# Optimization experiments

Hardware: AMD Instinct MI355X
Metric: run time of the kernel (lower is better)

## Reference

```python
import jax, jax.numpy as jnp
import numpy as np

N, T, V = 256, 70, 64
B, H, C = 6, 1024, 4  # n_blocks, n_internal_units, n_class
SPECTRAL_RADIUS = 0.99
INPUT_SCALING = 0.2


def setup_inputs() -> dict:
    key = jax.random.key(0)
    k1, k2, k3, k4 = jax.random.split(key, 4)
    X = jax.random.normal(k1, (N, T, V), dtype=jnp.float32)
    # spectral-radius-normalized reservoir weights (circular law: rho(G/sqrt(H)) ~ 1)
    W_res = jax.random.normal(k2, (B, H, H), dtype=jnp.float32) * (SPECTRAL_RADIUS / jnp.sqrt(H).astype(jnp.float32))
    # +/-1 Bernoulli input weights scaled by input_scaling
    W_in = jnp.sign(jax.random.normal(k3, (B, H, V), dtype=jnp.float32)) * INPUT_SCALING
    W_lin = jax.random.normal(k4, (T, C, B * H), dtype=jnp.float32) * 0.02
    b_lin = jnp.zeros((T, C), dtype=jnp.float32)
    return {"X": X, "W_res": W_res, "W_in": W_in, "W_lin": W_lin, "b_lin": b_lin}


def reference(X, W_res, W_in, W_lin, b_lin):
    # Echo state recurrence: s_t = tanh(W_res @ s_{t-1} + W_in @ x_t), per block
    # (leak=None, noise_level=0.0, n_drop=0 as in module defaults)
    n, t_len, v = X.shape
    b, h, _ = W_res.shape

    def step(s, x_t):  # s: [B,N,H], x_t: [N,V]
        pre = jnp.einsum('bij,bnj->bni', W_res, s) + jnp.einsum('bhv,nv->bnh', W_in, x_t)
        s_new = jnp.tanh(pre)
        return s_new, s_new

    s0 = jnp.zeros((b, n, h), dtype=X.dtype)
    _, states = jax.lax.scan(step, s0, jnp.swapaxes(X, 0, 1))  # [T,B,N,H]

    # per-timestep features: concat blocks -> [T,N,B*H]
    feats = jnp.transpose(states, (0, 2, 1, 3)).reshape(t_len, n, b * h)
    # per-timestep linear heads
    logits = jnp.einsum('tnf,tcf->tnc', feats, W_lin) + b_lin[:, None, :]  # [T,N,C]
    preds = jnp.argmax(logits, axis=-1)  # [T,N], matches forward()'s class_dict
    return logits, preds
```

## Files before the change

kernel.cpp:

```cpp
#include <hip/hip_runtime.h>
#include <stdint.h>


typedef _Float16 f16;
typedef _Float16 f16x8 __attribute__((ext_vector_type(8)));
typedef float floatx4 __attribute__((ext_vector_type(4)));

#define N_TOT 256
#define T_TOT 70
#define V_TOT 64
#define B_TOT 6
#define H_TOT 1024
#define C_TOT 4
#define F_TOT (B_TOT * H_TOT)
#define G_TOT 192
#define LDA 72
#define LO_SCALE 4096.0f
#define LO_INV   (1.0f / 4096.0f)

union H8 { f16 h[8]; uint4 v; };

__global__ __launch_bounds__(256)
void split_f32(const float* __restrict__ src, f16* __restrict__ hi,
               f16* __restrict__ lo, int n)
{
    const int i = (blockIdx.x * 256 + threadIdx.x) * 8;
    if (i + 8 > n) return;
    const float4 a = *(const float4*)&src[i];
    const float4 b = *(const float4*)&src[i + 4];
    const float x[8] = {a.x, a.y, a.z, a.w, b.x, b.y, b.z, b.w};
    H8 H, L;
#pragma unroll
    for (int j = 0; j < 8; ++j) {
        const f16 h = (f16)x[j];
        H.h[j] = h;
        L.h[j] = (f16)((x[j] - (float)h) * LO_SCALE);
    }
    *(uint4*)&hi[i] = H.v;
    *(uint4*)&lo[i] = L.v;
}

__global__ __launch_bounds__(256)
void head_reduce(const float* __restrict__ part,
                 const float* __restrict__ b_lin,
                 float* __restrict__ logits,
                 float* __restrict__ preds)
{
    const int t = blockIdx.x;
    const int n = threadIdx.x;

    float a0 = b_lin[t * C_TOT + 0];
    float a1 = b_lin[t * C_TOT + 1];
    float a2 = b_lin[t * C_TOT + 2];
    float a3 = b_lin[t * C_TOT + 3];

    const float* p = part + (((size_t)t * G_TOT) * N_TOT + n) * C_TOT;
    for (int g = 0; g < G_TOT; ++g) {
        const float4 v = *(const float4*)&p[(size_t)g * N_TOT * C_TOT];
        a0 += v.x; a1 += v.y; a2 += v.z; a3 += v.w;
    }

    float4 o = {a0, a1, a2, a3};
    *(float4*)&logits[((size_t)t * N_TOT + n) * C_TOT] = o;

    int arg = 0;
    float best = a0;
    if (a1 > best) { best = a1; arg = 1; }
    if (a2 > best) { best = a2; arg = 2; }
    if (a3 > best) { best = a3; arg = 3; }
    preds[(size_t)t * N_TOT + n] = (float)arg;
}

__global__ __launch_bounds__(256)
void esn_step_fused(const f16* __restrict__ Xhi,   const f16* __restrict__ Xlo,
                    const f16* __restrict__ Whi,   const f16* __restrict__ Wlo,
                    const f16* __restrict__ Wihi,  const f16* __restrict__ Wilo,
                    const f16* __restrict__ shi_p, const f16* __restrict__ slo_p,
                    f16* __restrict__ shi_n,       f16* __restrict__ slo_n,
                    const float* __restrict__ W_lin, float* __restrict__ part,
                    int t, int first)
{
    __shared__ f16 As_hi[64 * LDA];
    __shared__ f16 As_lo[64 * LDA];
    __shared__ f16 Bs_hi[32 * LDA];
    __shared__ f16 Bs_lo[32 * LDA];

    const int p   = blockIdx.x;
    const int l   = (p & 7) * 96 + (p >> 3);
    const int mt  = l & 3;
    const int bi  = l >> 2;
    const int b   = bi >> 5;
    const int it  = bi & 31;

    const int tid  = threadIdx.x;
    const int wm   = tid >> 6;
    const int lane = tid & 63;
    const int l16  = lane & 15;
    const int oct  = lane >> 4;

    const int ra = tid >> 2;
    const int ca = (tid & 3) << 4;
    const int rb = tid >> 3;
    const int cb = (tid & 7) << 3;

    floatx4 acc[2], accl[2];
#pragma unroll
    for (int j = 0; j < 2; ++j) { acc[j] = (floatx4)(0.0f); accl[j] = (floatx4)(0.0f); }

    if (!first) {
        const f16* Ah = shi_p + (size_t)(b * N_TOT + mt * 64 + ra) * H_TOT + ca;
        const f16* Al = slo_p + (size_t)(b * N_TOT + mt * 64 + ra) * H_TOT + ca;
        const f16* Bh = Whi   + (size_t)(b * H_TOT + it * 32 + rb) * H_TOT + cb;
        const f16* Bl = Wlo   + (size_t)(b * H_TOT + it * 32 + rb) * H_TOT + cb;

        uint4 pah0, pah1, pal0, pal1, pbh, pbl;
#define LOAD_CHUNK(J0)                                   \
        do {                                             \
            pah0 = *(const uint4*)&Ah[(J0) + 0];         \
            pah1 = *(const uint4*)&Ah[(J0) + 8];         \
            pal0 = *(const uint4*)&Al[(J0) + 0];         \
            pal1 = *(const uint4*)&Al[(J0) + 8];         \
            pbh  = *(const uint4*)&Bh[(J0)];             \
            pbl  = *(const uint4*)&Bl[(J0)];             \
        } while (0)

        LOAD_CHUNK(0);
        for (int kc = 0; kc < 16; ++kc) {
            if (kc) __syncthreads();
            *(uint4*)&As_hi[ra * LDA + ca]     = pah0;
            *(uint4*)&As_hi[ra * LDA + ca + 8] = pah1;
            *(uint4*)&As_lo[ra * LDA + ca]     = pal0;
            *(uint4*)&As_lo[ra * LDA + ca + 8] = pal1;
            *(uint4*)&Bs_hi[rb * LDA + cb]     = pbh;
            *(uint4*)&Bs_lo[rb * LDA + cb]     = pbl;
            __syncthreads();
            if (kc < 15) LOAD_CHUNK((kc + 1) * 64);

#pragma unroll
            for (int kk = 0; kk < 64; kk += 32) {
                const int ar = (wm * 16 + l16) * LDA + kk + oct * 8;
                const f16x8 ah = *(const f16x8*)&As_hi[ar];
                const f16x8 al = *(const f16x8*)&As_lo[ar];
#pragma unroll
                for (int nf = 0; nf < 2; ++nf) {
                    const int br = (nf * 16 + l16) * LDA + kk + oct * 8;
                    const f16x8 bh = *(const f16x8*)&Bs_hi[br];
                    const f16x8 bl = *(const f16x8*)&Bs_lo[br];
                    acc[nf]  = __builtin_amdgcn_mfma_f32_16x16x32_f16(ah, bh, acc[nf], 0, 0, 0);
                    accl[nf] = __builtin_amdgcn_mfma_f32_16x16x32_f16(ah, bl, accl[nf], 0, 0, 0);
                    accl[nf] = __builtin_amdgcn_mfma_f32_16x16x32_f16(al, bh, accl[nf], 0, 0, 0);
                }
            }
        }
#undef LOAD_CHUNK
        __syncthreads();
    }

    {
        const size_t xb = ((size_t)(mt * 64 + ra) * T_TOT + t) * V_TOT + ca;
        *(uint4*)&As_hi[ra * LDA + ca]     = *(const uint4*)&Xhi[xb];
        *(uint4*)&As_hi[ra * LDA + ca + 8] = *(const uint4*)&Xhi[xb + 8];
        *(uint4*)&As_lo[ra * LDA + ca]     = *(const uint4*)&Xlo[xb];
        *(uint4*)&As_lo[ra * LDA + ca + 8] = *(const uint4*)&Xlo[xb + 8];
        const size_t wb = (size_t)(b * H_TOT + it * 32 + rb) * V_TOT + cb;
        *(uint4*)&Bs_hi[rb * LDA + cb] = *(const uint4*)&Wihi[wb];
        *(uint4*)&Bs_lo[rb * LDA + cb] = *(const uint4*)&Wilo[wb];
        __syncthreads();
#pragma unroll
        for (int kk = 0; kk < 64; kk += 32) {
            const int ar = (wm * 16 + l16) * LDA + kk + oct * 8;
            const f16x8 ah = *(const f16x8*)&As_hi[ar];
            const f16x8 al = *(const f16x8*)&As_lo[ar];
#pragma unroll
            for (int nf = 0; nf < 2; ++nf) {
                const int br = (nf * 16 + l16) * LDA + kk + oct * 8;
                const f16x8 bh = *(const f16x8*)&Bs_hi[br];
                const f16x8 bl = *(const f16x8*)&Bs_lo[br];
                acc[nf]  = __builtin_amdgcn_mfma_f32_16x16x32_f16(ah, bh, acc[nf], 0, 0, 0);
                accl[nf] = __builtin_amdgcn_mfma_f32_16x16x32_f16(ah, bl, accl[nf], 0, 0, 0);
                accl[nf] = __builtin_amdgcn_mfma_f32_16x16x32_f16(al, bh, accl[nf], 0, 0, 0);
            }
        }
    }

    const int nbase = mt * 64;
    const int ibase = it * 32;

    const float* wl = W_lin + (size_t)t * C_TOT * F_TOT + b * H_TOT + ibase;
    float w[4][2];
#pragma unroll
    for (int c = 0; c < 4; ++c)
#pragma unroll
        for (int nf = 0; nf < 2; ++nf)
            w[c][nf] = wl[(size_t)c * F_TOT + nf * 16 + l16];

    float sval[2][4];
#pragma unroll
    for (int nf = 0; nf < 2; ++nf)
#pragma unroll
        for (int r = 0; r < 4; ++r) {
            const int m  = wm * 16 + oct * 4 + r;
            const int ii = nf * 16 + l16;
            const float s = tanhf(acc[nf][r] + accl[nf][r] * LO_INV);
            sval[nf][r] = s;
            const f16 h = (f16)s;
            const size_t oidx = (size_t)(b * N_TOT + nbase + m) * H_TOT + ibase + ii;
            shi_n[oidx] = h;
            slo_n[oidx] = (f16)((s - (float)h) * LO_SCALE);
        }

    const int g = b * 32 + it;
#pragma unroll
    for (int r = 0; r < 4; ++r) {
        float v[4];
#pragma unroll
        for (int c = 0; c < 4; ++c) {
            float x = sval[0][r] * w[c][0] + sval[1][r] * w[c][1];
            x += __shfl_xor(x, 1);
            x += __shfl_xor(x, 2);
            x += __shfl_xor(x, 4);
            x += __shfl_xor(x, 8);
            v[c] = x;
        }
        if (l16 == 0) {
            const int n = nbase + wm * 16 + oct * 4 + r;
            float4 o = {v[0], v[1], v[2], v[3]};
            *(float4*)&part[(((size_t)t * G_TOT + g) * N_TOT + n) * C_TOT] = o;
        }
    }
}

extern "C" void kernel_launch(void* const* d_in, const int* in_sizes, int n_in,
                              void* d_out, int out_size, void* d_ws, size_t ws_size,
                              hipStream_t stream) {
    const float* X     = (const float*)d_in[0];
    const float* W_res = (const float*)d_in[1];
    const float* W_in  = (const float*)d_in[2];
    const float* W_lin = (const float*)d_in[3];
    const float* b_lin = (const float*)d_in[4];

    float* out    = (float*)d_out;
    float* logits = out;
    float* preds  = out + (size_t)T_TOT * N_TOT * C_TOT;

    const size_t nWres = (size_t)B_TOT * H_TOT * H_TOT;
    const size_t nWin  = (size_t)B_TOT * H_TOT * V_TOT;
    const size_t nX    = (size_t)N_TOT * T_TOT * V_TOT;
    const size_t nS    = (size_t)B_TOT * N_TOT * H_TOT;

    f16* p    = (f16*)d_ws;
    f16* Whi  = p;  p += nWres;
    f16* Wlo  = p;  p += nWres;
    f16* Wihi = p;  p += nWin;
    f16* Wilo = p;  p += nWin;
    f16* Xhi  = p;  p += nX;
    f16* Xlo  = p;  p += nX;
    f16* sAh  = p;  p += nS;
    f16* sAl  = p;  p += nS;
    f16* sBh  = p;  p += nS;
    f16* sBl  = p;  p += nS;
    float* part = (float*)p;

    split_f32<<<(int)(nWres / 2048), 256, 0, stream>>>(W_res, Whi, Wlo, (int)nWres);
    split_f32<<<(int)(nWin  / 2048), 256, 0, stream>>>(W_in, Wihi, Wilo, (int)nWin);
    split_f32<<<(int)(nX    / 2048), 256, 0, stream>>>(X, Xhi, Xlo, (int)nX);

    for (int t = 0; t < T_TOT; ++t) {
        const f16 *ph, *pl;
        f16 *nh, *nl;
        if (t & 1) { ph = sBh; pl = sBl; nh = sAh; nl = sAl; }
        else       { ph = sAh; pl = sAl; nh = sBh; nl = sBl; }
        esn_step_fused<<<B_TOT * 4 * 32, 256, 0, stream>>>(
            Xhi, Xlo, Whi, Wlo, Wihi, Wilo, ph, pl, nh, nl,
            W_lin, part, t, t == 0 ? 1 : 0);
    }
    head_reduce<<<T_TOT, 256, 0, stream>>>(part, b_lin, logits, preds);
}
```

Measured before the change: 1.744 ms.

## Enlarge per-block tile to 64x64 with 2x2 warp layout in ESN step

Each workgroup now computes a 64 (batch) x 64 (hidden) output tile instead of 64x32, with four waves arranged 2x2 and each wave holding a 2x2 grid of MFMA accumulators. This halves the grid to 384 blocks and increases register reuse of A and B fragments, cutting redundant loads of the state matrix from global memory. The trade-off is fewer blocks than before (384 on a 256-CU part) and higher register/LDS use per block, which may reduce occupancy and load balance.

```diff
diff --git a/kernel.cpp b/kernel.cpp
--- a/kernel.cpp
+++ b/kernel.cpp
@@ -82,46 +82,53 @@
 {
     __shared__ f16 As_hi[64 * LDA];
     __shared__ f16 As_lo[64 * LDA];
-    __shared__ f16 Bs_hi[32 * LDA];
-    __shared__ f16 Bs_lo[32 * LDA];
+    __shared__ f16 Bs_hi[64 * LDA];
+    __shared__ f16 Bs_lo[64 * LDA];
 
     const int p   = blockIdx.x;
-    const int l   = (p & 7) * 96 + (p >> 3);
+    const int l   = (p & 7) * 48 + (p >> 3);
     const int mt  = l & 3;
     const int bi  = l >> 2;
-    const int b   = bi >> 5;
-    const int it  = bi & 31;
+    const int b   = bi >> 4;
+    const int it  = bi & 15;
 
     const int tid  = threadIdx.x;
-    const int wm   = tid >> 6;
+    const int wq   = tid >> 6;
+    const int wr   = wq >> 1;
+    const int wc   = wq & 1;
     const int lane = tid & 63;
     const int l16  = lane & 15;
     const int oct  = lane >> 4;
 
     const int ra = tid >> 2;
     const int ca = (tid & 3) << 4;
-    const int rb = tid >> 3;
-    const int cb = (tid & 7) << 3;
-
-    floatx4 acc[2], accl[2];
-#pragma unroll
-    for (int j = 0; j < 2; ++j) { acc[j] = (floatx4)(0.0f); accl[j] = (floatx4)(0.0f); }
+
+    floatx4 acc[2][2], accl[2][2];
+#pragma unroll
+    for (int m = 0; m < 2; ++m)
+#pragma unroll
+        for (int nf = 0; nf < 2; ++nf) {
+            acc[m][nf] = (floatx4)(0.0f);
+            accl[m][nf] = (floatx4)(0.0f);
+        }
 
     if (!first) {
         const f16* Ah = shi_p + (size_t)(b * N_TOT + mt * 64 + ra) * H_TOT + ca;
         const f16* Al = slo_p + (size_t)(b * N_TOT + mt * 64 + ra) * H_TOT + ca;
-        const f16* Bh = Whi   + (size_t)(b * H_TOT + it * 32 + rb) * H_TOT + cb;
-        const f16* Bl = Wlo   + (size_t)(b * H_TOT + it * 32 + rb) * H_TOT + cb;
-
-        uint4 pah0, pah1, pal0, pal1, pbh, pbl;
+        const f16* Bh = Whi   + (size_t)(b * H_TOT + it * 64 + ra) * H_TOT + ca;
+        const f16* Bl = Wlo   + (size_t)(b * H_TOT + it * 64 + ra) * H_TOT + ca;
+
+        uint4 pah0, pah1, pal0, pal1, pbh0, pbh1, pbl0, pbl1;
 #define LOAD_CHUNK(J0)                                   \
         do {                                             \
             pah0 = *(const uint4*)&Ah[(J0) + 0];         \
             pah1 = *(const uint4*)&Ah[(J0) + 8];         \
             pal0 = *(const uint4*)&Al[(J0) + 0];         \
             pal1 = *(const uint4*)&Al[(J0) + 8];         \
-            pbh  = *(const uint4*)&Bh[(J0)];             \
-            pbl  = *(const uint4*)&Bl[(J0)];             \
+            pbh0 = *(const uint4*)&Bh[(J0) + 0];         \
+            pbh1 = *(const uint4*)&Bh[(J0) + 8];         \
+            pbl0 = *(const uint4*)&Bl[(J0) + 0];         \
+            pbl1 = *(const uint4*)&Bl[(J0) + 8];         \
         } while (0)
 
         LOAD_CHUNK(0);
@@ -131,24 +138,33 @@
             *(uint4*)&As_hi[ra * LDA + ca + 8] = pah1;
             *(uint4*)&As_lo[ra * LDA + ca]     = pal0;
             *(uint4*)&As_lo[ra * LDA + ca + 8] = pal1;
-            *(uint4*)&Bs_hi[rb * LDA + cb]     = pbh;
-            *(uint4*)&Bs_lo[rb * LDA + cb]     = pbl;
+            *(uint4*)&Bs_hi[ra * LDA + ca]     = pbh0;
+            *(uint4*)&Bs_hi[ra * LDA + ca + 8] = pbh1;
+            *(uint4*)&Bs_lo[ra * LDA + ca]     = pbl0;
+            *(uint4*)&Bs_lo[ra * LDA + ca + 8] = pbl1;
             __syncthreads();
             if (kc < 15) LOAD_CHUNK((kc + 1) * 64);
 
 #pragma unroll
             for (int kk = 0; kk < 64; kk += 32) {
-                const int ar = (wm * 16 + l16) * LDA + kk + oct * 8;
-                const f16x8 ah = *(const f16x8*)&As_hi[ar];
-                const f16x8 al = *(const f16x8*)&As_lo[ar];
+                f16x8 ah[2], al[2];
+#pragma unroll
+                for (int m = 0; m < 2; ++m) {
+                    const int ar = (wr * 32 + m * 16 + l16) * LDA + kk + oct * 8;
+                    ah[m] = *(const f16x8*)&As_hi[ar];
+                    al[m] = *(const f16x8*)&As_lo[ar];
+                }
 #pragma unroll
                 for (int nf = 0; nf < 2; ++nf) {
-                    const int br = (nf * 16 + l16) * LDA + kk + oct * 8;
+                    const int br = (wc * 32 + nf * 16 + l16) * LDA + kk + oct * 8;
                     const f16x8 bh = *(const f16x8*)&Bs_hi[br];
                     const f16x8 bl = *(const f16x8*)&Bs_lo[br];
-                    acc[nf]  = __builtin_amdgcn_mfma_f32_16x16x32_f16(ah, bh, acc[nf], 0, 0, 0);
-                    accl[nf] = __builtin_amdgcn_mfma_f32_16x16x32_f16(ah, bl, accl[nf], 0, 0, 0);
-                    accl[nf] = __builtin_amdgcn_mfma_f32_16x16x32_f16(al, bh, accl[nf], 0, 0, 0);
+#pragma unroll
+                    for (int m = 0; m < 2; ++m) {
+                        acc[m][nf]  = __builtin_amdgcn_mfma_f32_16x16x32_f16(ah[m], bh, acc[m][nf], 0, 0, 0);
+                        accl[m][nf] = __builtin_amdgcn_mfma_f32_16x16x32_f16(ah[m], bl, accl[m][nf], 0, 0, 0);
+                        accl[m][nf] = __builtin_amdgcn_mfma_f32_16x16x32_f16(al[m], bh, accl[m][nf], 0, 0, 0);
+                    }
                 }
             }
         }
@@ -162,29 +178,38 @@
         *(uint4*)&As_hi[ra * LDA + ca + 8] = *(const uint4*)&Xhi[xb + 8];
         *(uint4*)&As_lo[ra * LDA + ca]     = *(const uint4*)&Xlo[xb];
         *(uint4*)&As_lo[ra * LDA + ca + 8] = *(const uint4*)&Xlo[xb + 8];
-        const size_t wb = (size_t)(b * H_TOT + it * 32 + rb) * V_TOT + cb;
-        *(uint4*)&Bs_hi[rb * LDA + cb] = *(const uint4*)&Wihi[wb];
-        *(uint4*)&Bs_lo[rb * LDA + cb] = *(const uint4*)&Wilo[wb];
+        const size_t wb = (size_t)(b * H_TOT + it * 64 + ra) * V_TOT + ca;
+        *(uint4*)&Bs_hi[ra * LDA + ca]     = *(const uint4*)&Wihi[wb];
+        *(uint4*)&Bs_hi[ra * LDA + ca + 8] = *(const uint4*)&Wihi[wb + 8];
+        *(uint4*)&Bs_lo[ra * LDA + ca]     = *(const uint4*)&Wilo[wb];
+        *(uint4*)&Bs_lo[ra * LDA + ca + 8] = *(const uint4*)&Wilo[wb + 8];
         __syncthreads();
 #pragma unroll
         for (int kk = 0; kk < 64; kk += 32) {
-            const int ar = (wm * 16 + l16) * LDA + kk + oct * 8;
-            const f16x8 ah = *(const f16x8*)&As_hi[ar];
-            const f16x8 al = *(const f16x8*)&As_lo[ar];
+            f16x8 ah[2], al[2];
+#pragma unroll
+            for (int m = 0; m < 2; ++m) {
+                const int ar = (wr * 32 + m * 16 + l16) * LDA + kk + oct * 8;
+                ah[m] = *(const f16x8*)&As_hi[ar];
+                al[m] = *(const f16x8*)&As_lo[ar];
+            }
 #pragma unroll
             for (int nf = 0; nf < 2; ++nf) {
-                const int br = (nf * 16 + l16) * LDA + kk + oct * 8;
+                const int br = (wc * 32 + nf * 16 + l16) * LDA + kk + oct * 8;
                 const f16x8 bh = *(const f16x8*)&Bs_hi[br];
                 const f16x8 bl = *(const f16x8*)&Bs_lo[br];
-                acc[nf]  = __builtin_amdgcn_mfma_f32_16x16x32_f16(ah, bh, acc[nf], 0, 0, 0);
-                accl[nf] = __builtin_amdgcn_mfma_f32_16x16x32_f16(ah, bl, accl[nf], 0, 0, 0);
-                accl[nf] = __builtin_amdgcn_mfma_f32_16x16x32_f16(al, bh, accl[nf], 0, 0, 0);
+#pragma unroll
+                for (int m = 0; m < 2; ++m) {
+                    acc[m][nf]  = __builtin_amdgcn_mfma_f32_16x16x32_f16(ah[m], bh, acc[m][nf], 0, 0, 0);
+                    accl[m][nf] = __builtin_amdgcn_mfma_f32_16x16x32_f16(ah[m], bl, accl[m][nf], 0, 0, 0);
+                    accl[m][nf] = __builtin_amdgcn_mfma_f32_16x16x32_f16(al[m], bh, accl[m][nf], 0, 0, 0);
+                }
             }
         }
     }
 
     const int nbase = mt * 64;
-    const int ibase = it * 32;
+    const int ibase = it * 64;
 
     const float* wl = W_lin + (size_t)t * C_TOT * F_TOT + b * H_TOT + ibase;
     float w[4][2];
@@ -192,42 +217,46 @@
     for (int c = 0; c < 4; ++c)
 #pragma unroll
         for (int nf = 0; nf < 2; ++nf)
-            w[c][nf] = wl[(size_t)c * F_TOT + nf * 16 + l16];
-
-    float sval[2][4];
-#pragma unroll
-    for (int nf = 0; nf < 2; ++nf)
+            w[c][nf] = wl[(size_t)c * F_TOT + wc * 32 + nf * 16 + l16];
+
+    float sval[2][2][4];
+#pragma unroll
+    for (int m = 0; m < 2; ++m)
+#pragma unroll
+        for (int nf = 0; nf < 2; ++nf)
+#pragma unroll
+            for (int r = 0; r < 4; ++r) {
+                const int mrow = wr * 32 + m * 16 + oct * 4 + r;
+                const int ii   = wc * 32 + nf * 16 + l16;
+                const float s = tanhf(acc[m][nf][r] + accl[m][nf][r] * LO_INV);
+                sval[m][nf][r] = s;
+                const f16 h = (f16)s;
+                const size_t oidx = (size_t)(b * N_TOT + nbase + mrow) * H_TOT + ibase + ii;
+                shi_n[oidx] = h;
+                slo_n[oidx] = (f16)((s - (float)h) * LO_SCALE);
+            }
+
+    const int g = b * 32 + it * 2 + wc;
+#pragma unroll
+    for (int m = 0; m < 2; ++m)
 #pragma unroll
         for (int r = 0; r < 4; ++r) {
-            const int m  = wm * 16 + oct * 4 + r;
-            const int ii = nf * 16 + l16;
-            const float s = tanhf(acc[nf][r] + accl[nf][r] * LO_INV);
-            sval[nf][r] = s;
-            const f16 h = (f16)s;
-            const size_t oidx = (size_t)(b * N_TOT + nbase + m) * H_TOT + ibase + ii;
-            shi_n[oidx] = h;
-            slo_n[oidx] = (f16)((s - (float)h) * LO_SCALE);
+            float v[4];
+#pragma unroll
+            for (int c = 0; c < 4; ++c) {
+                float x = sval[m][0][r] * w[c][0] + sval[m][1][r] * w[c][1];
+                x += __shfl_xor(x, 1);
+                x += __shfl_xor(x, 2);
+                x += __shfl_xor(x, 4);
+                x += __shfl_xor(x, 8);
+                v[c] = x;
+            }
+            if (l16 == 0) {
+                const int n = nbase + wr * 32 + m * 16 + oct * 4 + r;
+                float4 o = {v[0], v[1], v[2], v[3]};
+                *(float4*)&part[(((size_t)t * G_TOT + g) * N_TOT + n) * C_TOT] = o;
+            }
         }
-
-    const int g = b * 32 + it;
-#pragma unroll
-    for (int r = 0; r < 4; ++r) {
-        float v[4];
-#pragma unroll
-        for (int c = 0; c < 4; ++c) {
-            float x = sval[0][r] * w[c][0] + sval[1][r] * w[c][1];
-            x += __shfl_xor(x, 1);
-            x += __shfl_xor(x, 2);
-            x += __shfl_xor(x, 4);
-            x += __shfl_xor(x, 8);
-            v[c] = x;
-        }
-        if (l16 == 0) {
-            const int n = nbase + wm * 16 + oct * 4 + r;
-            float4 o = {v[0], v[1], v[2], v[3]};
-            *(float4*)&part[(((size_t)t * G_TOT + g) * N_TOT + n) * C_TOT] = o;
-        }
-    }
 }
 
 extern "C" void kernel_launch(void* const* d_in, const int* in_sizes, int n_in,
@@ -270,7 +299,7 @@
         f16 *nh, *nl;
         if (t & 1) { ph = sBh; pl = sBl; nh = sAh; nl = sAl; }
         else       { ph = sAh; pl = sAl; nh = sBh; nl = sBl; }
-        esn_step_fused<<<B_TOT * 4 * 32, 256, 0, stream>>>(
+        esn_step_fused<<<B_TOT * 16 * 4, 256, 0, stream>>>(
             Xhi, Xlo, Whi, Wlo, Wihi, Wilo, ph, pl, nh, nl,
             W_lin, part, t, t == 0 ? 1 : 0);
     }
```

Result: slower. 1.834 ms (+5.2%).

## Stream GEMM tiles via direct global-to-LDS loads with double-buffered swizzled LDS

Applied to the files above, without the earlier changes.

Replaces register-staged global loads plus LDS stores with `global_load_lds` 16-byte direct transfers into two LDS buffers. This overlaps the next K-chunk's load with the current chunk's MFMA work and cuts one barrier per iteration. Padding rows to LDA 72 gives way to an XOR swizzle of 8-element chunks, to avoid bank conflicts without wasting LDS. The input-projection tile becomes a 17th pipeline stage in the same loop. The costs are a doubled LDS footprint and reliance on the compiler inserting the right waitcnt before barriers for the async LDS writes.

```diff
diff --git a/kernel.cpp b/kernel.cpp
--- a/kernel.cpp
+++ b/kernel.cpp
@@ -14,11 +14,15 @@
 #define C_TOT 4
 #define F_TOT (B_TOT * H_TOT)
 #define G_TOT 192
-#define LDA 72
 #define LO_SCALE 4096.0f
 #define LO_INV   (1.0f / 4096.0f)
 
 union H8 { f16 h[8]; uint4 v; };
+
+#define GLOAD16(g, l)                                                        \
+    __builtin_amdgcn_global_load_lds(                                        \
+        (const __attribute__((address_space(1))) void*)(g),                  \
+        (__attribute__((address_space(3))) void*)(l), 16, 0, 0)
 
 __global__ __launch_bounds__(256)
 void split_f32(const float* __restrict__ src, f16* __restrict__ hi,
@@ -80,10 +84,10 @@
                     const float* __restrict__ W_lin, float* __restrict__ part,
                     int t, int first)
 {
-    __shared__ f16 As_hi[64 * LDA];
-    __shared__ f16 As_lo[64 * LDA];
-    __shared__ f16 Bs_hi[32 * LDA];
-    __shared__ f16 Bs_lo[32 * LDA];
+    __shared__ f16 As_hi[2][64 * 64];
+    __shared__ f16 As_lo[2][64 * 64];
+    __shared__ f16 Bs_hi[2][32 * 64];
+    __shared__ f16 Bs_lo[2][32 * 64];
 
     const int p   = blockIdx.x;
     const int l   = (p & 7) * 96 + (p >> 3);
@@ -93,113 +97,111 @@
     const int it  = bi & 31;
 
     const int tid  = threadIdx.x;
-    const int wm   = tid >> 6;
+    const int w    = tid >> 6;
     const int lane = tid & 63;
     const int l16  = lane & 15;
     const int oct  = lane >> 4;
-
-    const int ra = tid >> 2;
-    const int ca = (tid & 3) << 4;
-    const int rb = tid >> 3;
-    const int cb = (tid & 7) << 3;
+    const int r8   = lane >> 3;
+    const int sw   = ((lane & 7) ^ r8) << 3;
+
+    const int dA0 = (w * 16) * 64;
+    const int dA1 = (w * 16 + 8) * 64;
+    const int dB  = (w * 8) * 64;
+
+    const int arow0 = mt * 64 + w * 16 + r8;
+    const int arow1 = arow0 + 8;
+    const int brow  = it * 32 + w * 8 + r8;
+
+    const f16* Ah0 = shi_p + (size_t)(b * N_TOT + arow0) * H_TOT + sw;
+    const f16* Ah1 = shi_p + (size_t)(b * N_TOT + arow1) * H_TOT + sw;
+    const f16* Al0 = slo_p + (size_t)(b * N_TOT + arow0) * H_TOT + sw;
+    const f16* Al1 = slo_p + (size_t)(b * N_TOT + arow1) * H_TOT + sw;
+    const f16* Bh0 = Whi   + (size_t)(b * H_TOT + brow) * H_TOT + sw;
+    const f16* Bl0 = Wlo   + (size_t)(b * H_TOT + brow) * H_TOT + sw;
+    const f16* Xh0 = Xhi + ((size_t)arow0 * T_TOT + t) * V_TOT + sw;
+    const f16* Xh1 = Xhi + ((size_t)arow1 * T_TOT + t) * V_TOT + sw;
+    const f16* Xl0 = Xlo + ((size_t)arow0 * T_TOT + t) * V_TOT + sw;
+    const f16* Xl1 = Xlo + ((size_t)arow1 * T_TOT + t) * V_TOT + sw;
+    const f16* Wih = Wihi + (size_t)(b * H_TOT + brow) * V_TOT + sw;
+    const f16* Wil = Wilo + (size_t)(b * H_TOT + brow) * V_TOT + sw;
+
+    auto STAGE = [&](int k) {
+        const int bb = k & 1;
+        if (k < 16) {
+            const size_t off = (size_t)k * 64;
+            GLOAD16(Ah0 + off, &As_hi[bb][dA0]);
+            GLOAD16(Ah1 + off, &As_hi[bb][dA1]);
+            GLOAD16(Al0 + off, &As_lo[bb][dA0]);
+            GLOAD16(Al1 + off, &As_lo[bb][dA1]);
+            GLOAD16(Bh0 + off, &Bs_hi[bb][dB]);
+            GLOAD16(Bl0 + off, &Bs_lo[bb][dB]);
+        } else {
+            GLOAD16(Xh0, &As_hi[bb][dA0]);
+            GLOAD16(Xh1, &As_hi[bb][dA1]);
+            GLOAD16(Xl0, &As_lo[bb][dA0]);
+            GLOAD16(Xl1, &As_lo[bb][dA1]);
+            GLOAD16(Wih, &Bs_hi[bb][dB]);
+            GLOAD16(Wil, &Bs_lo[bb][dB]);
+        }
+    };
 
     floatx4 acc[2], accl[2];
 #pragma unroll
     for (int j = 0; j < 2; ++j) { acc[j] = (floatx4)(0.0f); accl[j] = (floatx4)(0.0f); }
 
-    if (!first) {
-        const f16* Ah = shi_p + (size_t)(b * N_TOT + mt * 64 + ra) * H_TOT + ca;
-        const f16* Al = slo_p + (size_t)(b * N_TOT + mt * 64 + ra) * H_TOT + ca;
-        const f16* Bh = Whi   + (size_t)(b * H_TOT + it * 32 + rb) * H_TOT + cb;
-        const f16* Bl = Wlo   + (size_t)(b * H_TOT + it * 32 + rb) * H_TOT + cb;
-
-        uint4 pah0, pah1, pal0, pal1, pbh, pbl;
-#define LOAD_CHUNK(J0)                                   \
-        do {                                             \
-            pah0 = *(const uint4*)&Ah[(J0) + 0];         \
-            pah1 = *(const uint4*)&Ah[(J0) + 8];         \
-            pal0 = *(const uint4*)&Al[(J0) + 0];         \
-            pal1 = *(const uint4*)&Al[(J0) + 8];         \
-            pbh  = *(const uint4*)&Bh[(J0)];             \
-            pbl  = *(const uint4*)&Bl[(J0)];             \
-        } while (0)
-
-        LOAD_CHUNK(0);
-        for (int kc = 0; kc < 16; ++kc) {
-            if (kc) __syncthreads();
-            *(uint4*)&As_hi[ra * LDA + ca]     = pah0;
-            *(uint4*)&As_hi[ra * LDA + ca + 8] = pah1;
-            *(uint4*)&As_lo[ra * LDA + ca]     = pal0;
-            *(uint4*)&As_lo[ra * LDA + ca + 8] = pal1;
-            *(uint4*)&Bs_hi[rb * LDA + cb]     = pbh;
-            *(uint4*)&Bs_lo[rb * LDA + cb]     = pbl;
-            __syncthreads();
-            if (kc < 15) LOAD_CHUNK((kc + 1) * 64);
-
-#pragma unroll
-            for (int kk = 0; kk < 64; kk += 32) {
-                const int ar = (wm * 16 + l16) * LDA + kk + oct * 8;
-                const f16x8 ah = *(const f16x8*)&As_hi[ar];
-                const f16x8 al = *(const f16x8*)&As_lo[ar];
-#pragma unroll
-                for (int nf = 0; nf < 2; ++nf) {
-                    const int br = (nf * 16 + l16) * LDA + kk + oct * 8;
-                    const f16x8 bh = *(const f16x8*)&Bs_hi[br];
-                    const f16x8 bl = *(const f16x8*)&Bs_lo[br];
-                    acc[nf]  = __builtin_amdgcn_mfma_f32_16x16x32_f16(ah, bh, acc[nf], 0, 0, 0);
-                    accl[nf] = __builtin_amdgcn_mfma_f32_16x16x32_f16(ah, bl, accl[nf], 0, 0, 0);
-                    accl[nf] = __builtin_amdgcn_mfma_f32_16x16x32_f16(al, bh, accl[nf], 0, 0, 0);
-                }
-            }
-        }
-#undef LOAD_CHUNK
-        __syncthreads();
-    }
-
-    {
-        const size_t xb = ((size_t)(mt * 64 + ra) * T_TOT + t) * V_TOT + ca;
-        *(uint4*)&As_hi[ra * LDA + ca]     = *(const uint4*)&Xhi[xb];
-        *(uint4*)&As_hi[ra * LDA + ca + 8] = *(const uint4*)&Xhi[xb + 8];
-        *(uint4*)&As_lo[ra * LDA + ca]     = *(const uint4*)&Xlo[xb];
-        *(uint4*)&As_lo[ra * LDA + ca + 8] = *(const uint4*)&Xlo[xb + 8];
-        const size_t wb = (size_t)(b * H_TOT + it * 32 + rb) * V_TOT + cb;
-        *(uint4*)&Bs_hi[rb * LDA + cb] = *(const uint4*)&Wihi[wb];
-        *(uint4*)&Bs_lo[rb * LDA + cb] = *(const uint4*)&Wilo[wb];
-        __syncthreads();
-#pragma unroll
-        for (int kk = 0; kk < 64; kk += 32) {
-            const int ar = (wm * 16 + l16) * LDA + kk + oct * 8;
-            const f16x8 ah = *(const f16x8*)&As_hi[ar];
-            const f16x8 al = *(const f16x8*)&As_lo[ar];
+    const int xsw = (l16 & 7) << 3;
+    const int aoff[2] = {
+        (w * 16 + l16) * 64 + ((0 + oct * 8) ^ xsw),
+        (w * 16 + l16) * 64 + ((32 + oct * 8) ^ xsw)
+    };
+    int boff[2][2];
+#pragma unroll
+    for (int nf = 0; nf < 2; ++nf) {
+        boff[nf][0] = (nf * 16 + l16) * 64 + ((0 + oct * 8) ^ xsw);
+        boff[nf][1] = (nf * 16 + l16) * 64 + ((32 + oct * 8) ^ xsw);
+    }
+
+    const int kc0 = first ? 16 : 0;
+    STAGE(kc0);
+    __syncthreads();
+
+    for (int kc = kc0; kc <= 16; ++kc) {
+        const int bb = kc & 1;
+        if (kc < 16) STAGE(kc + 1);
+
+#pragma unroll
+        for (int half = 0; half < 2; ++half) {
+            const f16x8 ah = *(const f16x8*)&As_hi[bb][aoff[half]];
+            const f16x8 al = *(const f16x8*)&As_lo[bb][aoff[half]];
 #pragma unroll
             for (int nf = 0; nf < 2; ++nf) {
-                const int br = (nf * 16 + l16) * LDA + kk + oct * 8;
-                const f16x8 bh = *(const f16x8*)&Bs_hi[br];
-                const f16x8 bl = *(const f16x8*)&Bs_lo[br];
+                const f16x8 bh = *(const f16x8*)&Bs_hi[bb][boff[nf][half]];
+                const f16x8 bl = *(const f16x8*)&Bs_lo[bb][boff[nf][half]];
                 acc[nf]  = __builtin_amdgcn_mfma_f32_16x16x32_f16(ah, bh, acc[nf], 0, 0, 0);
                 accl[nf] = __builtin_amdgcn_mfma_f32_16x16x32_f16(ah, bl, accl[nf], 0, 0, 0);
                 accl[nf] = __builtin_amdgcn_mfma_f32_16x16x32_f16(al, bh, accl[nf], 0, 0, 0);
             }
         }
+        if (kc < 16) __syncthreads();
     }
 
     const int nbase = mt * 64;
     const int ibase = it * 32;
 
     const float* wl = W_lin + (size_t)t * C_TOT * F_TOT + b * H_TOT + ibase;
-    float w[4][2];
+    float wv[4][2];
 #pragma unroll
     for (int c = 0; c < 4; ++c)
 #pragma unroll
         for (int nf = 0; nf < 2; ++nf)
-            w[c][nf] = wl[(size_t)c * F_TOT + nf * 16 + l16];
+            wv[c][nf] = wl[(size_t)c * F_TOT + nf * 16 + l16];
 
     float sval[2][4];
 #pragma unroll
     for (int nf = 0; nf < 2; ++nf)
 #pragma unroll
         for (int r = 0; r < 4; ++r) {
-            const int m  = wm * 16 + oct * 4 + r;
+            const int m  = w * 16 + oct * 4 + r;
             const int ii = nf * 16 + l16;
             const float s = tanhf(acc[nf][r] + accl[nf][r] * LO_INV);
             sval[nf][r] = s;
@@ -215,7 +217,7 @@
         float v[4];
 #pragma unroll
         for (int c = 0; c < 4; ++c) {
-            float x = sval[0][r] * w[c][0] + sval[1][r] * w[c][1];
+            float x = sval[0][r] * wv[c][0] + sval[1][r] * wv[c][1];
             x += __shfl_xor(x, 1);
             x += __shfl_xor(x, 2);
             x += __shfl_xor(x, 4);
@@ -223,7 +225,7 @@
             v[c] = x;
         }
         if (l16 == 0) {
-            const int n = nbase + wm * 16 + oct * 4 + r;
+            const int n = nbase + w * 16 + oct * 4 + r;
             float4 o = {v[0], v[1], v[2], v[3]};
             *(float4*)&part[(((size_t)t * G_TOT + g) * N_TOT + n) * C_TOT] = o;
         }
```

After: 1.511 ms. -13.3%, faster.
